# Kernel tuning notes

Hardware: AMD Instinct MI355X
Metric: run time of the kernel (lower is better)

Reference implementation:

```python
import jax, jax.numpy as jnp
import numpy as np

FEATURES = 8
POINTS = 3
CLASSES = 128
BATCH = 1024
TEMPERATURE = 0.1


def setup_inputs() -> dict:
    key = jax.random.key(0)
    k1, k2, k3 = jax.random.split(key, 3)
    x = jax.random.normal(k1, (BATCH, FEATURES), dtype=jnp.float32)
    beta = jax.random.uniform(k2, (FEATURES, POINTS), dtype=jnp.float32)
    classifier = jax.random.uniform(
        k3, ((POINTS + 1) ** FEATURES, CLASSES), dtype=jnp.float32)
    return {"x": x, "beta": beta, "classifier": classifier}


def reference(x, beta, classifier):
    # b: sort beta ascending per-feature, negate, cumsum, prepend a zero bin edge
    T = 1.0 / TEMPERATURE
    bneg = jnp.cumsum(-jnp.sort(beta, axis=1), axis=1)            # [F, P]
    b = jnp.concatenate(
        [jnp.zeros((beta.shape[0], 1), beta.dtype), bneg], axis=1)  # [F, P+1]
    w = jnp.arange(1, POINTS + 2, dtype=x.dtype)                  # [P+1]
    # soft one-hot binning per feature: [B, F, P+1]
    logits = (x[:, :, None] * w[None, None, :] + b[None, :, :]) * T
    hot = jax.nn.softmax(logits, axis=-1)
    # iterative outer product over features -> joint leaf histogram [B, (P+1)^F]
    B = x.shape[0]
    leaves = hot[:, 0, :]
    for f in range(1, FEATURES):  # small fixed loop over features
        leaves = (leaves[:, :, None] * hot[:, f, None, :]).reshape(B, -1)
    return leaves @ classifier  # [B, classes]
```

## Files before the change

kernel.cpp:

```cpp
#include <hip/hip_runtime.h>
#include <stdint.h>

typedef unsigned short u16;
typedef __attribute__((ext_vector_type(4))) float f32x4;
typedef __attribute__((ext_vector_type(2))) float f32x2;
typedef __attribute__((ext_vector_type(8))) short s16x8;

#define T_INV 10.0f
#define QEPS 9.5367431640625e-07f

__device__ __forceinline__ u16 f2bf(float f) {
  uint32_t u = __float_as_uint(f);
  uint32_t r = (u + 0x7FFFu + ((u >> 16) & 1u)) >> 16;
  return (u16)r;
}

__device__ __forceinline__ void gload_lds16(const void* g, void* l) {
  __builtin_amdgcn_global_load_lds(
      (const __attribute__((address_space(1))) uint32_t*)(g),
      (__attribute__((address_space(3))) uint32_t*)(l),
      16, 0, 0);
}

__global__ __launch_bounds__(256) void k_prep(
    const float* __restrict__ cls, const float* __restrict__ x,
    const float* __restrict__ beta,
    u16* __restrict__ ct, u16* __restrict__ plo, float* __restrict__ phiT)
{
  const int t = threadIdx.x;
  if (blockIdx.x < 1024) {
    __shared__ float tile[64 * 132];
    const int k0 = blockIdx.x * 64;
#pragma unroll
    for (int it = 0; it < 8; ++it) {
      int e = it * 1024 + t * 4;
      int r = e >> 7;
      int c = e & 127;
      f32x4 v = *(const f32x4*)(cls + (size_t)(k0 + r) * 128 + c);
      *(f32x4*)(tile + r * 132 + c) = v;
    }
    __syncthreads();
    const int c  = t >> 1;
    const int kh = t & 1;
    u16 vals[32];
#pragma unroll
    for (int j = 0; j < 32; ++j)
      vals[j] = f2bf(tile[(kh*32 + j) * 132 + c]);
    u16* dst = ct + ((size_t)(k0 >> 3) + kh * 4) * 1024 + c * 8;
#pragma unroll
    for (int qq = 0; qq < 4; ++qq) {
      s16x8 v;
#pragma unroll
      for (int e2 = 0; e2 < 8; ++e2) v[e2] = (short)vals[qq*8 + e2];
      *(s16x8*)(dst + (size_t)qq * 1024) = v;
    }
  } else {
    const int b = (blockIdx.x - 1024) * 64 + (t >> 2);
    const int q = t & 3;
    float hot[8][4];
#pragma unroll
    for (int f = 0; f < 8; ++f) {
      float b0 = beta[f*3+0], b1 = beta[f*3+1], b2 = beta[f*3+2];
      float s0 = fminf(b0, fminf(b1, b2));
      float s2 = fmaxf(b0, fmaxf(b1, b2));
      float s1 = b0 + b1 + b2 - s0 - s2;
      float bv1 = -s0, bv2 = -(s0 + s1), bv3 = -(s0 + s1 + s2);
      float xf = x[b*8 + f];
      float l0 = (xf * 1.0f       ) * T_INV;
      float l1 = (xf * 2.0f + bv1) * T_INV;
      float l2 = (xf * 3.0f + bv2) * T_INV;
      float l3 = (xf * 4.0f + bv3) * T_INV;
      float mm = fmaxf(fmaxf(l0, l1), fmaxf(l2, l3));
      float e0 = __expf(l0 - mm), e1 = __expf(l1 - mm);
      float e2 = __expf(l2 - mm), e3 = __expf(l3 - mm);
      float inv = 1.0f / (e0 + e1 + e2 + e3);
      hot[f][0] = e0*inv; hot[f][1] = e1*inv; hot[f][2] = e2*inv; hot[f][3] = e3*inv;
    }
    {
      float h23[16];
#pragma unroll
      for (int i2 = 0; i2 < 4; ++i2)
#pragma unroll
        for (int i3 = 0; i3 < 4; ++i3) h23[i2*4+i3] = hot[2][i2] * hot[3][i3];
      float h0q = hot[0][q];
#pragma unroll
      for (int i1 = 0; i1 < 4; ++i1) {
        float c01 = h0q * hot[1][i1];
#pragma unroll
        for (int j = 0; j < 16; ++j)
          phiT[(size_t)(q*64 + i1*16 + j) * 1024 + b] = c01 * h23[j];
      }
    }
    {
      float h67[16];
#pragma unroll
      for (int i6 = 0; i6 < 4; ++i6)
#pragma unroll
        for (int i7 = 0; i7 < 4; ++i7) h67[i6*4+i7] = hot[6][i6] * hot[7][i7];
      float h4q = hot[4][q];
      u16* dst = plo + (size_t)b*256 + q*64;
#pragma unroll
      for (int i5 = 0; i5 < 4; ++i5) {
        float c45 = h4q * hot[5][i5];
#pragma unroll
        for (int j = 0; j < 16; j += 8) {
          s16x8 v;
#pragma unroll
          for (int e = 0; e < 8; ++e) v[e] = (short)f2bf(c45 * h67[j+e]);
          *(s16x8*)(dst + i5*16 + j) = v;
        }
      }
    }
  }
}

__global__ __launch_bounds__(256, 2) void k_main(
    const u16* __restrict__ plo, const float* __restrict__ phiT,
    const u16* __restrict__ ct, u16* __restrict__ pws)
{
  __shared__ __align__(16) u16 As[32768];
  __shared__ __align__(16) u16 Bb[2][4096];

  const int wg  = blockIdx.x;
  const int xcd = wg & 7;
  const int idx = wg >> 3;
  const int hig = xcd * 8 + (idx >> 3);
  const int m   = idx & 7;

  const int t    = threadIdx.x;
  const int l    = t & 63;
  const int w    = t >> 6;
  const int lrow = l & 15;
  const int kg   = l >> 4;
  const int rbase = (w & 1) * 64;
  const int cbase = (w >> 1) * 64;

  const u16* ploM = plo + (size_t)m * 128 * 256;

#pragma unroll
  for (int i = 0; i < 16; ++i) {
    int ks  = i >> 1;
    int row = (i & 1) * 64 + (t >> 2);
    int g   = ((t & 3) - ((t >> 3) & 3)) & 3;
    gload_lds16(ploM + (size_t)row * 256 + ks * 32 + g * 8, &As[i * 2048 + t * 8]);
  }

  int aoff[4], boff[4];
#pragma unroll
  for (int mt = 0; mt < 4; ++mt) {
    int row = rbase + mt * 16 + lrow;
    aoff[mt] = row * 32 + (((kg + ((row >> 1) & 3)) & 3)) * 8;
  }
#pragma unroll
  for (int nt = 0; nt < 4; ++nt) {
    int c = cbase + nt * 16 + lrow;
    boff[nt] = c * 32 + (((kg + ((c >> 1) & 3)) & 3)) * 8;
  }

  const int bc = t & 127;
  const int bg = t >> 7;
  const u16* bsrc = ct + (size_t)hig * 131072 + (size_t)bc * 8
                       + (size_t)bg * 1024;
  const int s0 = (bg + ((bc >> 1) & 3)) & 3;
  const int s2 = ((bg + 2) + ((bc >> 1) & 3)) & 3;

  s16x8 bregE0, bregE1, bregO0, bregO1;
  bregE0 = *(const s16x8*)(bsrc + 0 * 4096);
  bregE1 = *(const s16x8*)(bsrc + 0 * 4096 + 2048);
  bregO0 = *(const s16x8*)(bsrc + 1 * 4096);
  bregO1 = *(const s16x8*)(bsrc + 1 * 4096 + 2048);
  *(s16x8*)(&Bb[0][bc * 32 + s0 * 8]) = bregE0;
  *(s16x8*)(&Bb[0][bc * 32 + s2 * 8]) = bregE1;
  __syncthreads();

  f32x4 qprev[4];
  {
    const float* p0 = phiT + (size_t)(hig * 4) * 1024 + m * 128;
#pragma unroll
    for (int mt = 0; mt < 4; ++mt) {
      f32x4 q = *(const f32x4*)(p0 + rbase + mt * 16 + kg * 4);
#pragma unroll
      for (int r = 0; r < 4; ++r) qprev[mt][r] = fmaxf(q[r], QEPS);
    }
  }

  f32x4 acc[4][4];
#pragma unroll
  for (int i = 0; i < 4; ++i)
#pragma unroll
    for (int j = 0; j < 4; ++j) acc[i][j] = (f32x4)0.0f;

  s16x8 afrP[4];
#pragma unroll
  for (int mt = 0; mt < 4; ++mt)
    afrP[mt] = *(const s16x8*)(&As[aoff[mt]]);

#pragma unroll 1
  for (int h = 0; h < 4; ++h) {
#pragma unroll
    for (int ks = 0; ks < 8; ++ks) {
      const int tt = h * 8 + ks;
      if (h < 3 || ks < 6) {
        const u16* p = bsrc + (size_t)(tt + 2) * 4096;
        if (ks & 1) { bregO0 = *(const s16x8*)p; bregO1 = *(const s16x8*)(p + 2048); }
        else        { bregE0 = *(const s16x8*)p; bregE1 = *(const s16x8*)(p + 2048); }
      }
      s16x8 bfr[4];
#pragma unroll
      for (int nt = 0; nt < 4; ++nt)
        bfr[nt] = *(const s16x8*)(&Bb[ks & 1][boff[nt]]);
      __builtin_amdgcn_s_setprio(1);
#pragma unroll
      for (int mt = 0; mt < 4; ++mt)
#pragma unroll
        for (int nt = 0; nt < 4; ++nt)
          acc[mt][nt] = __builtin_amdgcn_mfma_f32_16x16x32_bf16(
              afrP[mt], bfr[nt], acc[mt][nt], 0, 0, 0);
      __builtin_amdgcn_s_setprio(0);
      {
        const int nks = (ks + 1) & 7;
#pragma unroll
        for (int mt = 0; mt < 4; ++mt)
          afrP[mt] = *(const s16x8*)(&As[nks * 4096 + aoff[mt]]);
      }
      if (h < 3 || ks < 7) {
        u16* d = &Bb[(ks + 1) & 1][bc * 32];
        if (ks & 1) { *(s16x8*)(d + s0 * 8) = bregE0; *(s16x8*)(d + s2 * 8) = bregE1; }
        else        { *(s16x8*)(d + s0 * 8) = bregO0; *(s16x8*)(d + s2 * 8) = bregO1; }
      }
      asm volatile("s_waitcnt lgkmcnt(0)" ::: "memory");
      __builtin_amdgcn_sched_barrier(0);
      __builtin_amdgcn_s_barrier();
      __builtin_amdgcn_sched_barrier(0);
    }
    if (h < 3) {
      const float* pn = phiT + (size_t)(hig * 4 + h + 1) * 1024 + m * 128;
#pragma unroll
      for (int mt = 0; mt < 4; ++mt) {
        f32x4 qn = *(const f32x4*)(pn + rbase + mt * 16 + kg * 4);
        f32x4 ratio;
#pragma unroll
        for (int r = 0; r < 4; ++r) {
          float q = fmaxf(qn[r], QEPS);
          ratio[r] = qprev[mt][r] * __builtin_amdgcn_rcpf(q);
          qprev[mt][r] = q;
        }
#pragma unroll
        for (int nt = 0; nt < 4; ++nt)
#pragma unroll
          for (int r = 0; r < 4; ++r)
            acc[mt][nt][r] *= ratio[r];
      }
    }
  }

  __syncthreads();
  {
    u16* ob = As;
#pragma unroll
    for (int mt = 0; mt < 4; ++mt)
#pragma unroll
      for (int r = 0; r < 4; ++r) {
        int row = rbase + mt * 16 + kg * 4 + r;
#pragma unroll
        for (int nt = 0; nt < 4; ++nt) {
          int col = cbase + nt * 16 + lrow;
          ob[row * 136 + col] = f2bf(acc[mt][nt][r] * qprev[mt][r]);
        }
      }
    __syncthreads();
    const int row  = t >> 1;
    const int half = t & 1;
    const u16* srcp = ob + row * 136 + half * 64;
    u16* gdst = pws + ((size_t)hig * 1024 + (size_t)m * 128) * 128
                    + row * 128 + half * 64;
#pragma unroll
    for (int i = 0; i < 8; ++i)
      *(s16x8*)(gdst + i * 8) = *(const s16x8*)(srcp + i * 8);
  }
}

__global__ __launch_bounds__(256) void k_reduce(
    const u16* __restrict__ p, float* __restrict__ out)
{
  const int g = blockIdx.x * 256 + threadIdx.x;
  const u16* src = p + (size_t)g * 2;
  float a0 = 0.0f, a1 = 0.0f;
#pragma unroll 8
  for (int hig = 0; hig < 64; ++hig) {
    uint32_t v = *(const uint32_t*)(src + (size_t)hig * 131072);
    a0 += __uint_as_float((v & 0xFFFFu) << 16);
    a1 += __uint_as_float(v & 0xFFFF0000u);
  }
  f32x2 o; o.x = a0; o.y = a1;
  *(f32x2*)(out + (size_t)g * 2) = o;
}

extern "C" void kernel_launch(void* const* d_in, const int* in_sizes, int n_in,
                              void* d_out, int out_size, void* d_ws, size_t ws_size,
                              hipStream_t stream)
{
  const float* x    = (const float*)d_in[0];
  const float* beta = (const float*)d_in[1];
  const float* cls  = (const float*)d_in[2];
  float* out = (float*)d_out;

  char* ws = (char*)d_ws;
  u16*   ct   = (u16*)ws;
  u16*   plo  = (u16*)(ws + (16u << 20));
  float* phiT = (float*)(ws + (16u << 20) + 524288);
  u16*   pws  = (u16*)(ws + (16u << 20) + 524288 + 1048576);

  k_prep<<<1040, 256, 0, stream>>>(cls, x, beta, ct, plo, phiT);
  k_main<<<512, 256, 0, stream>>>(plo, phiT, ct, pws);
  k_reduce<<<256, 256, 0, stream>>>(pws, out);
}
```

Measured before the change: 45.79 us.

## Stage B tiles via direct global-to-LDS loads in four-step double-buffered chunks

Replaces the per-k-step register round trip for classifier tiles with global_load_lds DMA straight into a larger double-buffered LDS region holding four k-steps at a time. Barriers drop from one per k-step to one per four-step chunk, and B fragments are now prefetched into registers one step ahead. LDS use grows from 16 KB to 64 KB for B, so the launch-bounds occupancy hint of 2 is removed. This risks fewer resident workgroups per CU and less latency hiding.

```diff
diff --git a/kernel.cpp b/kernel.cpp
--- a/kernel.cpp
+++ b/kernel.cpp
@@ -114,12 +114,12 @@
   }
 }
 
-__global__ __launch_bounds__(256, 2) void k_main(
+__global__ __launch_bounds__(256) void k_main(
     const u16* __restrict__ plo, const float* __restrict__ phiT,
     const u16* __restrict__ ct, u16* __restrict__ pws)
 {
   __shared__ __align__(16) u16 As[32768];
-  __shared__ __align__(16) u16 Bb[2][4096];
+  __shared__ __align__(16) u16 Bh[2][16384];
 
   const int wg  = blockIdx.x;
   const int xcd = wg & 7;
@@ -157,21 +157,21 @@
     boff[nt] = c * 32 + (((kg + ((c >> 1) & 3)) & 3)) * 8;
   }
 
-  const int bc = t & 127;
-  const int bg = t >> 7;
-  const u16* bsrc = ct + (size_t)hig * 131072 + (size_t)bc * 8
-                       + (size_t)bg * 1024;
-  const int s0 = (bg + ((bc >> 1) & 3)) & 3;
-  const int s2 = ((bg + 2) + ((bc >> 1) & 3)) & 3;
-
-  s16x8 bregE0, bregE1, bregO0, bregO1;
-  bregE0 = *(const s16x8*)(bsrc + 0 * 4096);
-  bregE1 = *(const s16x8*)(bsrc + 0 * 4096 + 2048);
-  bregO0 = *(const s16x8*)(bsrc + 1 * 4096);
-  bregO1 = *(const s16x8*)(bsrc + 1 * 4096 + 2048);
-  *(s16x8*)(&Bb[0][bc * 32 + s0 * 8]) = bregE0;
-  *(s16x8*)(&Bb[0][bc * 32 + s2 * 8]) = bregE1;
-  __syncthreads();
+  auto stageB = [&](int p, int buf) {
+#pragma unroll
+    for (int i = 0; i < 8; ++i) {
+      int c = i * 16 + (l >> 2);
+      int g = ((l & 3) - ((c >> 1) & 3)) & 3;
+      gload_lds16(ct + (((size_t)(hig * 128 + p * 16 + w * 4 + g)) << 10) + c * 8,
+                  &Bh[buf][(w * 8 + i) * 512 + l * 8]);
+    }
+  };
+
+  stageB(0, 0);
+  asm volatile("s_waitcnt vmcnt(0)" ::: "memory");
+  __builtin_amdgcn_sched_barrier(0);
+  __builtin_amdgcn_s_barrier();
+  __builtin_amdgcn_sched_barrier(0);
 
   f32x4 qprev[4];
   {
@@ -190,51 +190,41 @@
 #pragma unroll
     for (int j = 0; j < 4; ++j) acc[i][j] = (f32x4)0.0f;
 
-  s16x8 afrP[4];
-#pragma unroll
-  for (int mt = 0; mt < 4; ++mt)
-    afrP[mt] = *(const s16x8*)(&As[aoff[mt]]);
+  s16x8 afrP[4], bfrC[4];
+#pragma unroll
+  for (int mt = 0; mt < 4; ++mt) afrP[mt] = *(const s16x8*)(&As[aoff[mt]]);
+#pragma unroll
+  for (int nt = 0; nt < 4; ++nt) bfrC[nt] = *(const s16x8*)(&Bh[0][boff[nt]]);
 
 #pragma unroll 1
-  for (int h = 0; h < 4; ++h) {
-#pragma unroll
-    for (int ks = 0; ks < 8; ++ks) {
-      const int tt = h * 8 + ks;
-      if (h < 3 || ks < 6) {
-        const u16* p = bsrc + (size_t)(tt + 2) * 4096;
-        if (ks & 1) { bregO0 = *(const s16x8*)p; bregO1 = *(const s16x8*)(p + 2048); }
-        else        { bregE0 = *(const s16x8*)p; bregE1 = *(const s16x8*)(p + 2048); }
-      }
-      s16x8 bfr[4];
-#pragma unroll
-      for (int nt = 0; nt < 4; ++nt)
-        bfr[nt] = *(const s16x8*)(&Bb[ks & 1][boff[nt]]);
+  for (int p = 0; p < 8; ++p) {
+    if (p < 7) stageB(p + 1, (p + 1) & 1);
+    const u16* Bcur = &Bh[p & 1][0];
+    const int ksb = (p & 1) * 4;
+#pragma unroll
+    for (int s = 0; s < 4; ++s) {
       __builtin_amdgcn_s_setprio(1);
 #pragma unroll
       for (int mt = 0; mt < 4; ++mt)
 #pragma unroll
         for (int nt = 0; nt < 4; ++nt)
           acc[mt][nt] = __builtin_amdgcn_mfma_f32_16x16x32_bf16(
-              afrP[mt], bfr[nt], acc[mt][nt], 0, 0, 0);
+              afrP[mt], bfrC[nt], acc[mt][nt], 0, 0, 0);
       __builtin_amdgcn_s_setprio(0);
       {
-        const int nks = (ks + 1) & 7;
+        const int nks = (ksb + s + 1) & 7;
 #pragma unroll
         for (int mt = 0; mt < 4; ++mt)
           afrP[mt] = *(const s16x8*)(&As[nks * 4096 + aoff[mt]]);
       }
-      if (h < 3 || ks < 7) {
-        u16* d = &Bb[(ks + 1) & 1][bc * 32];
-        if (ks & 1) { *(s16x8*)(d + s0 * 8) = bregE0; *(s16x8*)(d + s2 * 8) = bregE1; }
-        else        { *(s16x8*)(d + s0 * 8) = bregO0; *(s16x8*)(d + s2 * 8) = bregO1; }
-      }
-      asm volatile("s_waitcnt lgkmcnt(0)" ::: "memory");
-      __builtin_amdgcn_sched_barrier(0);
-      __builtin_amdgcn_s_barrier();
-      __builtin_amdgcn_sched_barrier(0);
-    }
-    if (h < 3) {
-      const float* pn = phiT + (size_t)(hig * 4 + h + 1) * 1024 + m * 128;
+      if (s < 3) {
+#pragma unroll
+        for (int nt = 0; nt < 4; ++nt)
+          bfrC[nt] = *(const s16x8*)(Bcur + (s + 1) * 4096 + boff[nt]);
+      }
+    }
+    if ((p & 1) && p < 7) {
+      const float* pn = phiT + (size_t)(hig * 4 + (p >> 1) + 1) * 1024 + m * 128;
 #pragma unroll
       for (int mt = 0; mt < 4; ++mt) {
         f32x4 qn = *(const f32x4*)(pn + rbase + mt * 16 + kg * 4);
@@ -251,6 +241,15 @@
           for (int r = 0; r < 4; ++r)
             acc[mt][nt][r] *= ratio[r];
       }
+    }
+    if (p < 7) {
+      asm volatile("s_waitcnt vmcnt(0)" ::: "memory");
+      __builtin_amdgcn_sched_barrier(0);
+      __builtin_amdgcn_s_barrier();
+      __builtin_amdgcn_sched_barrier(0);
+#pragma unroll
+      for (int nt = 0; nt < 4; ++nt)
+        bfrC[nt] = *(const s16x8*)(&Bh[(p + 1) & 1][boff[nt]]);
     }
   }
 
```

New measurement: 63.42 us. 1.39x slower.

## Double k_main workgroup to 512 threads with 8 waves each owning 64x32 tiles

Applied to the files above, without the earlier changes.

Changes the main GEMM kernel from 4 waves per workgroup, each computing a 64x64 output tile, to 8 waves each computing 64x32. The A-tile LDS fill, B staging loads and output copy loops are redistributed across 512 threads, and the accumulator count per wave is halved. The aim is more waves in flight to hide LDS and global latency, at the cost of each A fragment being reused over fewer MFMAs and more LDS reads per FLOP.

```diff
diff --git a/kernel.cpp b/kernel.cpp
--- a/kernel.cpp
+++ b/kernel.cpp
@@ -114,7 +114,7 @@
   }
 }
 
-__global__ __launch_bounds__(256, 2) void k_main(
+__global__ __launch_bounds__(512, 4) void k_main(
     const u16* __restrict__ plo, const float* __restrict__ phiT,
     const u16* __restrict__ ct, u16* __restrict__ pws)
 {
@@ -132,27 +132,26 @@
   const int w    = t >> 6;
   const int lrow = l & 15;
   const int kg   = l >> 4;
-  const int rbase = (w & 1) * 64;
-  const int cbase = (w >> 1) * 64;
+  const int rbase = (w >> 2) * 64;
+  const int cbase = (w & 3) * 32;
 
   const u16* ploM = plo + (size_t)m * 128 * 256;
 
 #pragma unroll
-  for (int i = 0; i < 16; ++i) {
-    int ks  = i >> 1;
-    int row = (i & 1) * 64 + (t >> 2);
+  for (int i = 0; i < 8; ++i) {
+    int row = t >> 2;
     int g   = ((t & 3) - ((t >> 3) & 3)) & 3;
-    gload_lds16(ploM + (size_t)row * 256 + ks * 32 + g * 8, &As[i * 2048 + t * 8]);
-  }
-
-  int aoff[4], boff[4];
+    gload_lds16(ploM + (size_t)row * 256 + i * 32 + g * 8, &As[i * 4096 + t * 8]);
+  }
+
+  int aoff[4], boff[2];
 #pragma unroll
   for (int mt = 0; mt < 4; ++mt) {
     int row = rbase + mt * 16 + lrow;
     aoff[mt] = row * 32 + (((kg + ((row >> 1) & 3)) & 3)) * 8;
   }
 #pragma unroll
-  for (int nt = 0; nt < 4; ++nt) {
+  for (int nt = 0; nt < 2; ++nt) {
     int c = cbase + nt * 16 + lrow;
     boff[nt] = c * 32 + (((kg + ((c >> 1) & 3)) & 3)) * 8;
   }
@@ -161,16 +160,12 @@
   const int bg = t >> 7;
   const u16* bsrc = ct + (size_t)hig * 131072 + (size_t)bc * 8
                        + (size_t)bg * 1024;
-  const int s0 = (bg + ((bc >> 1) & 3)) & 3;
-  const int s2 = ((bg + 2) + ((bc >> 1) & 3)) & 3;
-
-  s16x8 bregE0, bregE1, bregO0, bregO1;
-  bregE0 = *(const s16x8*)(bsrc + 0 * 4096);
-  bregE1 = *(const s16x8*)(bsrc + 0 * 4096 + 2048);
-  bregO0 = *(const s16x8*)(bsrc + 1 * 4096);
-  bregO1 = *(const s16x8*)(bsrc + 1 * 4096 + 2048);
-  *(s16x8*)(&Bb[0][bc * 32 + s0 * 8]) = bregE0;
-  *(s16x8*)(&Bb[0][bc * 32 + s2 * 8]) = bregE1;
+  const int sB = (bg + ((bc >> 1) & 3)) & 3;
+
+  s16x8 bregE, bregO;
+  bregE = *(const s16x8*)(bsrc + 0 * 4096);
+  bregO = *(const s16x8*)(bsrc + 1 * 4096);
+  *(s16x8*)(&Bb[0][bc * 32 + sB * 8]) = bregE;
   __syncthreads();
 
   f32x4 qprev[4];
@@ -184,11 +179,11 @@
     }
   }
 
-  f32x4 acc[4][4];
+  f32x4 acc[4][2];
 #pragma unroll
   for (int i = 0; i < 4; ++i)
 #pragma unroll
-    for (int j = 0; j < 4; ++j) acc[i][j] = (f32x4)0.0f;
+    for (int j = 0; j < 2; ++j) acc[i][j] = (f32x4)0.0f;
 
   s16x8 afrP[4];
 #pragma unroll
@@ -202,18 +197,18 @@
       const int tt = h * 8 + ks;
       if (h < 3 || ks < 6) {
         const u16* p = bsrc + (size_t)(tt + 2) * 4096;
-        if (ks & 1) { bregO0 = *(const s16x8*)p; bregO1 = *(const s16x8*)(p + 2048); }
-        else        { bregE0 = *(const s16x8*)p; bregE1 = *(const s16x8*)(p + 2048); }
-      }
-      s16x8 bfr[4];
-#pragma unroll
-      for (int nt = 0; nt < 4; ++nt)
+        if (ks & 1) bregO = *(const s16x8*)p;
+        else        bregE = *(const s16x8*)p;
+      }
+      s16x8 bfr[2];
+#pragma unroll
+      for (int nt = 0; nt < 2; ++nt)
         bfr[nt] = *(const s16x8*)(&Bb[ks & 1][boff[nt]]);
       __builtin_amdgcn_s_setprio(1);
 #pragma unroll
       for (int mt = 0; mt < 4; ++mt)
 #pragma unroll
-        for (int nt = 0; nt < 4; ++nt)
+        for (int nt = 0; nt < 2; ++nt)
           acc[mt][nt] = __builtin_amdgcn_mfma_f32_16x16x32_bf16(
               afrP[mt], bfr[nt], acc[mt][nt], 0, 0, 0);
       __builtin_amdgcn_s_setprio(0);
@@ -224,9 +219,8 @@
           afrP[mt] = *(const s16x8*)(&As[nks * 4096 + aoff[mt]]);
       }
       if (h < 3 || ks < 7) {
-        u16* d = &Bb[(ks + 1) & 1][bc * 32];
-        if (ks & 1) { *(s16x8*)(d + s0 * 8) = bregE0; *(s16x8*)(d + s2 * 8) = bregE1; }
-        else        { *(s16x8*)(d + s0 * 8) = bregO0; *(s16x8*)(d + s2 * 8) = bregO1; }
+        u16* d = &Bb[(ks + 1) & 1][bc * 32 + sB * 8];
+        *(s16x8*)d = (ks & 1) ? bregE : bregO;
       }
       asm volatile("s_waitcnt lgkmcnt(0)" ::: "memory");
       __builtin_amdgcn_sched_barrier(0);
@@ -246,7 +240,7 @@
           qprev[mt][r] = q;
         }
 #pragma unroll
-        for (int nt = 0; nt < 4; ++nt)
+        for (int nt = 0; nt < 2; ++nt)
 #pragma unroll
           for (int r = 0; r < 4; ++r)
             acc[mt][nt][r] *= ratio[r];
@@ -263,19 +257,19 @@
       for (int r = 0; r < 4; ++r) {
         int row = rbase + mt * 16 + kg * 4 + r;
 #pragma unroll
-        for (int nt = 0; nt < 4; ++nt) {
+        for (int nt = 0; nt < 2; ++nt) {
           int col = cbase + nt * 16 + lrow;
           ob[row * 136 + col] = f2bf(acc[mt][nt][r] * qprev[mt][r]);
         }
       }
     __syncthreads();
-    const int row  = t >> 1;
-    const int half = t & 1;
-    const u16* srcp = ob + row * 136 + half * 64;
+    const int row = t >> 2;
+    const int q4  = t & 3;
+    const u16* srcp = ob + row * 136 + q4 * 32;
     u16* gdst = pws + ((size_t)hig * 1024 + (size_t)m * 128) * 128
-                    + row * 128 + half * 64;
-#pragma unroll
-    for (int i = 0; i < 8; ++i)
+                    + row * 128 + q4 * 32;
+#pragma unroll
+    for (int i = 0; i < 4; ++i)
       *(s16x8*)(gdst + i * 8) = *(const s16x8*)(srcp + i * 8);
   }
 }
@@ -312,6 +306,6 @@
   u16*   pws  = (u16*)(ws + (16u << 20) + 524288 + 1048576);
 
   k_prep<<<1040, 256, 0, stream>>>(cls, x, beta, ct, plo, phiT);
-  k_main<<<512, 256, 0, stream>>>(plo, phiT, ct, pws);
+  k_main<<<512, 512, 0, stream>>>(plo, phiT, ct, pws);
   k_reduce<<<256, 256, 0, stream>>>(pws, out);
 }
```

Measured after the change: 46.72 us. +2.0%, slower.
